# Kernel optimization log

Measured on AMD Instinct MI355X. Metric: run time of the kernel, lower is better.

## Reference

```python
import jax, jax.numpy as jnp
import numpy as np

B, N, K, G = 8, 2048, 20, 8
EPS = 1e-5

def lrelu(v):
    return jnp.where(v >= 0, v, 0.2 * v)

def group_norm(x, gamma, beta):
    # x: (B, C, ...); normalize over channel groups and spatial dims
    b, c = x.shape[0], x.shape[1]
    xg = x.reshape(b, G, c // G, -1)
    mu = xg.mean(axis=(2, 3), keepdims=True)
    var = xg.var(axis=(2, 3), keepdims=True)
    xn = ((xg - mu) * jax.lax.rsqrt(var + EPS)).reshape(x.shape)
    sh = (1, c) + (1,) * (x.ndim - 2)
    return xn * gamma.reshape(sh) + beta.reshape(sh)

def graph_feature(x, k):
    # x: (B, C, N) -> edge features (B, 2C, N, k)
    inner = 2.0 * jnp.einsum('bcn,bcm->bnm', x, x)
    xx = jnp.sum(x * x, axis=1)                     # (B, N)
    pd = -(xx[:, :, None] - inner + xx[:, None, :]) # negative squared dist
    idx = jax.lax.top_k(pd, k)[1]                   # (B, N, k) nearest
    xt = jnp.swapaxes(x, 1, 2)                      # (B, N, C)
    nbr = jax.vmap(lambda f, i: f[i])(xt, idx)      # (B, N, k, C) gather
    ctr = jnp.broadcast_to(xt[:, :, None, :], nbr.shape)
    feat = jnp.concatenate([nbr - ctr, ctr], axis=-1)  # (B, N, k, 2C)
    return jnp.transpose(feat, (0, 3, 1, 2))

def edge_block(x, w, b, g, h):
    f = graph_feature(x, K)
    y = jnp.einsum('oc,bcnk->bonk', w, f) + b[None, :, None, None]
    return lrelu(group_norm(y, g, h)).max(axis=-1)   # (B, out, N)

def _forward(x, w0, b0, g0, h0, w1, b1, g1, h1, w2, b2, g2, h2,
             w3, b3, g3, h3, fw0, fb0, fw1, fb1, fw2, fb2):
    cur = jnp.swapaxes(x, 1, 2)                      # (B, 3, N)
    res = []
    for (w, b, g, h) in ((w0, b0, g0, h0), (w1, b1, g1, h1), (w2, b2, g2, h2)):
        cur = edge_block(cur, w, b, g, h)
        res.append(cur)
    xc = jnp.concatenate(res, axis=1)                # (B, 256, N)
    pf = jnp.einsum('oc,bcn->bon', w3, xc) + b3[None, :, None]
    pf = lrelu(group_norm(pf, g3, h3))               # (B, 256, N)
    v = jnp.concatenate([pf.max(axis=-1), pf.mean(axis=-1)], axis=1)  # (B, 512)
    v = lrelu(v @ fw0.T + fb0)
    v = lrelu(v @ fw1.T + fb1)
    return v @ fw2.T + fb2                           # (B, 256)

def setup_inputs():
    key = jax.random.key(0)
    ks = jax.random.split(key, 16)
    def rn(k, shape, s=0.05):
        return jax.random.normal(k, shape, jnp.float32) * s
    inp = {'x': jax.random.normal(ks[0], (B, N, 3), jnp.float32)}
    inp.update(w0=rn(ks[1], (64, 6)), b0=rn(ks[2], (64,)), g0=jnp.ones((64,)), h0=jnp.zeros((64,)))
    inp.update(w1=rn(ks[3], (64, 128)), b1=rn(ks[4], (64,)), g1=jnp.ones((64,)), h1=jnp.zeros((64,)))
    inp.update(w2=rn(ks[5], (128, 128)), b2=rn(ks[6], (128,)), g2=jnp.ones((128,)), h2=jnp.zeros((128,)))
    inp.update(w3=rn(ks[7], (256, 256)), b3=rn(ks[8], (256,)), g3=jnp.ones((256,)), h3=jnp.zeros((256,)))
    inp.update(fw0=rn(ks[9], (512, 512)), fb0=rn(ks[10], (512,)))
    inp.update(fw1=rn(ks[11], (512, 512)), fb1=rn(ks[12], (512,)))
    inp.update(fw2=rn(ks[13], (256, 512)), fb2=rn(ks[14], (256,)))
    return inp

def reference(x, w0, b0, g0, h0, w1, b1, g1, h1, w2, b2, g2, h2,
              w3, b3, g3, h3, fw0, fb0, fw1, fb1, fw2, fb2):
    return _forward(x, w0, b0, g0, h0, w1, b1, g1, h1, w2, b2, g2, h2,
                    w3, b3, g3, h3, fw0, fb0, fw1, fb1, fw2, fb2)
```

## Files before the change

### kernel.cpp

```cpp
#include <hip/hip_runtime.h>
#include <hip/hip_bf16.h>
#include <cstdint>


constexpr int B = 8, N = 2048, KNN = 20, G = 8;
constexpr int BN = B * N;
constexpr float EPS = 1e-5f;

using bf16 = __hip_bfloat16;
using u64 = unsigned long long;

__device__ __forceinline__ float lrelu(float v){ return v >= 0.f ? v : 0.2f * v; }
__device__ __forceinline__ unsigned fenc(float f){ unsigned u = __float_as_uint(f); return (u & 0x80000000u) ? ~u : (u | 0x80000000u); }
__device__ __forceinline__ float fdec(unsigned u){ return (u & 0x80000000u) ? __uint_as_float(u & 0x7FFFFFFFu) : __uint_as_float(~u); }

template<int NB>
__device__ __forceinline__ void batcher_sort(unsigned* s){
  #pragma unroll
  for (int p = 1; p < NB; p <<= 1){
    #pragma unroll
    for (int k = p; k >= 1; k >>= 1){
      #pragma unroll
      for (int j = k % p; j <= NB-1-k; j += 2*k){
        #pragma unroll
        for (int i = 0; i <= ((k-1 < NB-1-j-k) ? k-1 : NB-1-j-k); ++i){
          if ((i + j) / (2*p) == (i + j + k) / (2*p)){
            const unsigned lo = min(s[i+j], s[i+j+k]);
            const unsigned hi = max(s[i+j], s[i+j+k]);
            s[i+j] = lo; s[i+j+k] = hi;
          }
        }
      }
    }
  }
}

template<int NB>
__device__ __forceinline__ void topk_update(unsigned* L, const unsigned* s){
  #pragma unroll
  for (int i = 0; i < NB; ++i) L[i] = min(L[i], s[i]);
  #pragma unroll
  for (int gap = 16; gap >= 1; gap >>= 1){
    #pragma unroll
    for (int i = 0; i < 32; ++i){
      if ((i & ((gap<<1)-1)) < gap){
        const unsigned hi = max(L[i], L[i+gap]);
        const unsigned lo = min(L[i], L[i+gap]);
        L[i] = hi; L[i+gap] = lo;
      }
    }
  }
}

__device__ __forceinline__ u64 knn_dec8(unsigned kk, int q){
  const unsigned ord = kk & 255u;
  const unsigned gidx = (ord >> 4)*128u + (unsigned)q + 8u*(ord & 15u);
  return ((u64)(kk & 0xFFFFFF00u) << 24) | gidx;
}

__device__ __forceinline__ void knn_merge32(unsigned char* ovl, const unsigned* L,
    int* __restrict__ knn_out, size_t bp, int r0, int sr, int sq){
  unsigned* mbuf = (unsigned*)ovl;
  #pragma unroll
  for (int k = 0; k < KNN; ++k) mbuf[(sr*8 + sq)*KNN + k] = L[31-k];
  __syncthreads();
  if (sq == 0){
    int h[8]; u64 v[8];
    #pragma unroll
    for (int q = 0; q < 8; ++q){ h[q] = 0; v[q] = knn_dec8(mbuf[(sr*8+q)*KNN], q); }
    int* outp = &knn_out[(bp + r0 + sr)*KNN];
    for (int k = 0; k < KNN; ++k){
      int best = 0; u64 bv = v[0];
      #pragma unroll
      for (int q = 1; q < 8; ++q) if (v[q] < bv){ bv = v[q]; best = q; }
      outp[k] = (int)(unsigned)(bv & 0xFFFFu);
      #pragma unroll
      for (int q = 0; q < 8; ++q) if (q == best){
        ++h[q];
        v[q] = (h[q] < KNN) ? knn_dec8(mbuf[(sr*8+q)*KNN + h[q]], q) : ~0ULL;
      }
    }
  }
}

struct SrcPtrs { const void* p[23]; };

__global__ __launch_bounds__(256) void convert_kernel(SrcPtrs sp, float* __restrict__ dst,
                                                      float* gstat, unsigned* vmax, float* vmean){
  if (blockIdx.y == 23){
    int t = blockIdx.x * 256 + threadIdx.x;
    if (t < 512) gstat[t] = 0.f;
    if (t < B*256){ vmax[t] = 0x007FFFFFu; vmean[t] = 0.f; }
    return;
  }
  constexpr int CNT[23] = {49152,384,64,64,64,8192,64,64,64,16384,128,128,128,
                           65536,256,256,256,262144,512,262144,512,131072,256};
  constexpr int OFF[23] = {0,49152,49536,49600,49664,49728,57920,57984,58048,58112,
                           74496,74624,74752,74880,140416,140672,140928,141184,
                           403328,403840,665984,666496,797568};
  const int ti = blockIdx.y;
  const int cnt = CNT[ti], off = OFF[ti];
  const unsigned g0w = *(const unsigned*)sp.p[3];
  const bool isbf = (g0w & 0xFFFFu) == 0x3F80u;
  const float* fs = (const float*)sp.p[ti];
  const unsigned short* bs = (const unsigned short*)sp.p[ti];
  for (int j = blockIdx.x*256 + threadIdx.x; j < cnt; j += gridDim.x*256){
    dst[off + j] = isbf ? __uint_as_float((unsigned)bs[j] << 16) : fs[j];
  }
}

template<int C>
__global__ __launch_bounds__(256) void sqnorm_cm(const float* __restrict__ f, float* __restrict__ cn){
  const int p = blockIdx.x*256 + threadIdx.x;
  float s = 0.f;
  #pragma unroll 8
  for (int c = 0; c < C; ++c){ const float v = f[(size_t)c*BN + p]; s += v*v; }
  cn[p] = s;
}

template<int C>
__global__ __launch_bounds__(256) void knn_kernel(const float* __restrict__ feat, const float* __restrict__ cnG,
                                                  int* __restrict__ knn_out){
  constexpr int ROWS = 32, CT = 128, DTP = 133;
  constexpr int COLF_BYTES = C*CT*4;
  constexpr int MERGE_BYTES = ROWS*8*KNN*4;
  constexpr int OVL = COLF_BYTES + ROWS*DTP*4;
  __shared__ __align__(16) unsigned char ovl[OVL];
  __shared__ __align__(16) float rowfT[C][ROWS];
  float* colfT = (float*)ovl;
  float* dbuf  = (float*)(ovl + COLF_BYTES);

  const int t = threadIdx.x;
  const int b = blockIdx.y;
  const int r0 = blockIdx.x * ROWS;
  const size_t bp = (size_t)b * N;
  const int rg = (t & 7)*4;
  const int cg = (t >> 3)*4;
  const int sr = t >> 3;
  const int sq = t & 7;
  const float rn = cnG[bp + r0 + sr];

  for (int i = t; i < C*(ROWS/4); i += 256){
    const int c = i >> 3, r4 = (i & 7)*4;
    *(float4*)&rowfT[c][r4] = *(const float4*)&feat[(size_t)c*BN + bp + r0 + r4];
  }

  unsigned L[32];
  #pragma unroll
  for (int k = 0; k < 32; ++k) L[k] = 0xFFFFFFFFu;

  for (int ct = 0; ct < N/CT; ++ct){
    const int m0 = ct * CT;
    __syncthreads();
    for (int i = t; i < C*(CT/4); i += 256){
      const int c = i >> 5, m4 = (i & 31)*4;
      *(float4*)&colfT[c*CT + m4] = *(const float4*)&feat[(size_t)c*BN + bp + m0 + m4];
    }
    const float4 cn4 = *(const float4*)&cnG[bp + m0 + cg];
    __syncthreads();

    float acc[4][4];
    #pragma unroll
    for (int i=0;i<4;i++){
      #pragma unroll
      for (int j=0;j<4;j++) acc[i][j]=0.f; }
    for (int c = 0; c < C; ++c){
      float4 ar = *(const float4*)&rowfT[c][rg];
      float4 cl = *(const float4*)&colfT[c*CT + cg];
      acc[0][0]+=ar.x*cl.x; acc[0][1]+=ar.x*cl.y; acc[0][2]+=ar.x*cl.z; acc[0][3]+=ar.x*cl.w;
      acc[1][0]+=ar.y*cl.x; acc[1][1]+=ar.y*cl.y; acc[1][2]+=ar.y*cl.z; acc[1][3]+=ar.y*cl.w;
      acc[2][0]+=ar.z*cl.x; acc[2][1]+=ar.z*cl.y; acc[2][2]+=ar.z*cl.z; acc[2][3]+=ar.z*cl.w;
      acc[3][0]+=ar.w*cl.x; acc[3][1]+=ar.w*cl.y; acc[3][2]+=ar.w*cl.z; acc[3][3]+=ar.w*cl.w;
    }
    #pragma unroll
    for (int i=0;i<4;i++){
      float4 s;
      s.x = cn4.x - 2.f*acc[i][0]; s.y = cn4.y - 2.f*acc[i][1];
      s.z = cn4.z - 2.f*acc[i][2]; s.w = cn4.w - 2.f*acc[i][3];
      *(float4*)&dbuf[(rg+i)*DTP + cg] = s;
    }
    __syncthreads();

    const float* drow = &dbuf[sr*DTP];
    unsigned s16[16];
    #pragma unroll
    for (int j = 0; j < 16; ++j){
      const float d = fmaxf(drow[sq + 8*j] + rn, 0.f);
      s16[j] = (__float_as_uint(d) & 0xFFFFFF00u) | (unsigned)(ct*16 + j);
    }
    batcher_sort<16>(s16);
    topk_update<16>(L, s16);
  }

  __syncthreads();
  knn_merge32(ovl, L, knn_out, bp, r0, sr, sq);
}

__global__ __launch_bounds__(256) void knn3_kernel(const float* __restrict__ x, int* __restrict__ knn_out){
  constexpr int ROWS = 32, CT = 128;
  constexpr int MERGE_BYTES = ROWS*8*KNN*4;
  __shared__ __align__(16) unsigned char ovl[MERGE_BYTES];
  float* cx = (float*)ovl;
  float* cy = cx + CT;
  float* cz = cy + CT;

  const int t = threadIdx.x;
  const int b = blockIdx.y;
  const int r0 = blockIdx.x * ROWS;
  const size_t bp = (size_t)b * N;
  const int sr = t >> 3, sq = t & 7;
  const float rx = x[(bp + r0 + sr)*3 + 0];
  const float ry = x[(bp + r0 + sr)*3 + 1];
  const float rz = x[(bp + r0 + sr)*3 + 2];

  unsigned L[32];
  #pragma unroll
  for (int k = 0; k < 32; ++k) L[k] = 0xFFFFFFFFu;

  for (int ct = 0; ct < N/CT; ++ct){
    __syncthreads();
    if (t < CT){
      const size_t q = (bp + ct*CT + t)*3;
      cx[t] = x[q]; cy[t] = x[q+1]; cz[t] = x[q+2];
    }
    __syncthreads();
    unsigned s16[16];
    #pragma unroll
    for (int j = 0; j < 16; ++j){
      const int m = sq + 8*j;
      const float dx = rx - cx[m], dy = ry - cy[m], dz = rz - cz[m];
      const float d = dx*dx + dy*dy + dz*dz;
      s16[j] = (__float_as_uint(d) & 0xFFFFFF00u) | (unsigned)(ct*16 + j);
    }
    batcher_sort<16>(s16);
    topk_update<16>(L, s16);
  }

  __syncthreads();
  knn_merge32(ovl, L, knn_out, bp, r0, sr, sq);
}

template<int C, int COUT, int MT, bool CM>
__global__ __launch_bounds__(256) void zu_kernel(const float* __restrict__ feat, const float* __restrict__ w,
                                                 const float* __restrict__ bias,
                                                 float* __restrict__ z, float* __restrict__ u){
  __shared__ __align__(16) float fT[C][MT+4];
  __shared__ __align__(16) float Wt[C][COUT+4];
  const int t = threadIdx.x;
  const size_t p0 = (size_t)blockIdx.x * MT;
  if constexpr (CM){
    for (int i = t; i < C*(MT/4); i += 256){
      const int c = i / (MT/4), m4 = (i % (MT/4))*4;
      float4 v = *(const float4*)&feat[(size_t)c*BN + p0 + m4];
      *(float4*)&fT[c][m4] = v;
    }
  } else {
    for (int i = t; i < MT*C; i += 256){ int m = i / C, c = i - m*C; fT[c][m] = feat[(p0+m)*C + c]; }
  }
  for (int i = t; i < COUT*C; i += 256){ int o = i / C, c = i - o*C; Wt[c][o] = w[o*(2*C) + c]; }
  __syncthreads();
  constexpr int MQ = MT/4;
  const int rq = t % MQ, oq = t / MQ;
  const int mm = rq*4, oo = oq*8;
  float acc[4][8];
  #pragma unroll
  for (int i=0;i<4;i++){
    #pragma unroll
    for (int j=0;j<8;j++) acc[i][j] = 0.f; }
  for (int c = 0; c < C; ++c){
    float fr[4], wv[8];
    { float4 v = *(const float4*)&fT[c][mm]; fr[0]=v.x; fr[1]=v.y; fr[2]=v.z; fr[3]=v.w; }
    { float4 v = *(const float4*)&Wt[c][oo];   wv[0]=v.x; wv[1]=v.y; wv[2]=v.z; wv[3]=v.w; }
    { float4 v = *(const float4*)&Wt[c][oo+4]; wv[4]=v.x; wv[5]=v.y; wv[6]=v.z; wv[7]=v.w; }
    #pragma unroll
    for (int i=0;i<4;i++){
      #pragma unroll
      for (int j=0;j<8;j++) acc[i][j] += fr[i]*wv[j];
    }
  }
  #pragma unroll
  for (int i=0;i<4;i++){
    float4 s0, s1;
    s0.x=acc[i][0]; s0.y=acc[i][1]; s0.z=acc[i][2]; s0.w=acc[i][3];
    s1.x=acc[i][4]; s1.y=acc[i][5]; s1.z=acc[i][6]; s1.w=acc[i][7];
    *(float4*)&z[(p0+mm+i)*COUT + oo]     = s0;
    *(float4*)&z[(p0+mm+i)*COUT + oo + 4] = s1;
  }
  __syncthreads();
  for (int i = t; i < COUT*C; i += 256){
    int o = i / C, c = i - o*C;
    Wt[c][o] = w[o*2*C + C + c] - w[o*2*C + c];
  }
  __syncthreads();
  #pragma unroll
  for (int i=0;i<4;i++){
    #pragma unroll
    for (int j=0;j<8;j++) acc[i][j] = 0.f; }
  for (int c = 0; c < C; ++c){
    float fr[4], wv[8];
    { float4 v = *(const float4*)&fT[c][mm]; fr[0]=v.x; fr[1]=v.y; fr[2]=v.z; fr[3]=v.w; }
    { float4 v = *(const float4*)&Wt[c][oo];   wv[0]=v.x; wv[1]=v.y; wv[2]=v.z; wv[3]=v.w; }
    { float4 v = *(const float4*)&Wt[c][oo+4]; wv[4]=v.x; wv[5]=v.y; wv[6]=v.z; wv[7]=v.w; }
    #pragma unroll
    for (int i=0;i<4;i++){
      #pragma unroll
      for (int j=0;j<8;j++) acc[i][j] += fr[i]*wv[j];
    }
  }
  float bb[8];
  #pragma unroll
  for (int j=0;j<8;j++) bb[j] = bias[oo+j];
  #pragma unroll
  for (int i=0;i<4;i++){
    float4 s0, s1;
    s0.x=acc[i][0]+bb[0]; s0.y=acc[i][1]+bb[1]; s0.z=acc[i][2]+bb[2]; s0.w=acc[i][3]+bb[3];
    s1.x=acc[i][4]+bb[4]; s1.y=acc[i][5]+bb[5]; s1.z=acc[i][6]+bb[6]; s1.w=acc[i][7]+bb[7];
    *(float4*)&u[(p0+mm+i)*COUT + oo]     = s0;
    *(float4*)&u[(p0+mm+i)*COUT + oo + 4] = s1;
  }
}

template<int COUT, bool MM>
__global__ __launch_bounds__(256) void edge_stats_kernel(const float* __restrict__ z, const float* __restrict__ u,
                                                         const int* __restrict__ knn, float* __restrict__ gstat,
                                                         float* __restrict__ emax, float* __restrict__ emin){
  constexpr int REPS = 256 / COUT;
  constexpr int PPT  = 16 / REPS;
  __shared__ float red[G*2];
  const int t = threadIdx.x;
  const int o = t % COUT, pr = t / COUT;
  const size_t base = (size_t)blockIdx.x * 16;
  const int b = (int)(base / N);
  if (t < G*2) red[t] = 0.f;
  __syncthreads();
  float s1 = 0.f, s2 = 0.f;
  for (int j = 0; j < PPT; ++j){
    const size_t p = base + pr + (size_t)j*REPS;
    const float uu = u[p*COUT + o];
    const int* kn = knn + p*KNN;
    float mx = -3.0e38f, mn = 3.0e38f;
    for (int k = 0; k < KNN; ++k){
      const int m = kn[k];
      const float y = z[((size_t)b*N + m)*COUT + o] + uu;
      s1 += y; s2 += y*y;
      mx = fmaxf(mx, y); mn = fminf(mn, y);
    }
    if constexpr (MM){
      emax[(size_t)o*BN + p] = mx;
      emin[(size_t)o*BN + p] = mn;
    }
  }
  const int g = o / (COUT/G);
  atomicAdd(&red[g*2+0], s1);
  atomicAdd(&red[g*2+1], s2);
  __syncthreads();
  if (t < G*2) atomicAdd(&gstat[b*(G*2) + t], red[t]);
}

template<int COUT>
__global__ __launch_bounds__(256) void edge_norm_mm(const float* __restrict__ emax, const float* __restrict__ emin,
    const float* __restrict__ gstat, const float* __restrict__ gamma, const float* __restrict__ beta,
    float* __restrict__ fout, float cntInv){
  const int o = blockIdx.y;
  const int p = blockIdx.x*1024 + threadIdx.x*4;
  const int b = p >> 11;
  const int g = o / (COUT/G);
  const float s1 = gstat[b*(G*2) + g*2 + 0];
  const float s2 = gstat[b*(G*2) + g*2 + 1];
  const float mu  = s1 * cntInv;
  const float var = s2 * cntInv - mu*mu;
  const float inv = rsqrtf(var + EPS);
  const float sc = gamma[o] * inv;
  const float sh = beta[o] - mu * sc;
  float4 mx = *(const float4*)&emax[(size_t)o*BN + p];
  float4 mn = *(const float4*)&emin[(size_t)o*BN + p];
  float4 r;
  r.x = lrelu(sc*(sc>=0.f?mx.x:mn.x)+sh);
  r.y = lrelu(sc*(sc>=0.f?mx.y:mn.y)+sh);
  r.z = lrelu(sc*(sc>=0.f?mx.z:mn.z)+sh);
  r.w = lrelu(sc*(sc>=0.f?mx.w:mn.w)+sh);
  *(float4*)&fout[(size_t)o*BN + p] = r;
}

template<int COUT>
__global__ __launch_bounds__(256) void edge_norm_kernel(const float* __restrict__ z, const float* __restrict__ u,
    const int* __restrict__ knn, const float* __restrict__ gstat,
    const float* __restrict__ gamma, const float* __restrict__ beta,
    float* __restrict__ fout, float cntInv){
  constexpr int REPS = 256 / COUT;
  constexpr int PPT  = 16 / REPS;
  const int t = threadIdx.x;
  const int o = t % COUT, pr = t / COUT;
  const size_t base = (size_t)blockIdx.x * 16;
  const int b = (int)(base / N);
  const int g = o / (COUT/G);
  const float s1 = gstat[b*(G*2) + g*2 + 0];
  const float s2 = gstat[b*(G*2) + g*2 + 1];
  const float mu  = s1 * cntInv;
  const float var = s2 * cntInv - mu*mu;
  const float inv = rsqrtf(var + EPS);
  const float sc = gamma[o] * inv;
  const float sh = beta[o] - mu * sc;
  for (int j = 0; j < PPT; ++j){
    const size_t p = base + pr + (size_t)j*REPS;
    const float uu = u[p*COUT + o];
    const int* kn = knn + p*KNN;
    float mx = -3.0e38f;
    for (int k = 0; k < KNN; ++k){
      const int m = kn[k];
      const float y = z[((size_t)b*N + m)*COUT + o] + uu;
      mx = fmaxf(mx, lrelu(sc*y + sh));
    }
    fout[(size_t)o*BN + p] = mx;
  }
}

__global__ __launch_bounds__(256) void conv3_kernel(const float* __restrict__ f1, const float* __restrict__ f2,
    const float* __restrict__ f3, const float* __restrict__ w3, const float* __restrict__ b3,
    float* __restrict__ y3, float* __restrict__ gstat){
  __shared__ __align__(16) float fT[32][64+4];
  __shared__ __align__(16) float Wt[32][256+4];
  __shared__ float red[G*2];
  const int t = threadIdx.x;
  const size_t p0 = (size_t)blockIdx.x * 64;
  const int b = (int)(p0 / N);
  const int rq = t & 15, oq = t >> 4;
  const int mm = rq*4, oo = oq*16;
  if (t < G*2) red[t] = 0.f;
  float acc[4][16];
  #pragma unroll
  for (int i=0;i<4;i++){
    #pragma unroll
    for (int j=0;j<16;j++) acc[i][j] = 0.f; }
  for (int cc = 0; cc < 8; ++cc){
    __syncthreads();
    const float* src; int coff;
    if (cc < 2){ src = f1; coff = cc*32; }
    else if (cc < 4){ src = f2; coff = (cc-2)*32; }
    else { src = f3; coff = (cc-4)*32; }
    for (int i = t; i < 512; i += 256){
      const int c = i >> 4, m4 = (i & 15)*4;
      float4 v = *(const float4*)&src[(size_t)(coff+c)*BN + p0 + m4];
      *(float4*)&fT[c][m4] = v;
    }
    for (int i = t; i < 2048; i += 256){
      int o = i >> 3, cq = (i & 7)*4;
      float4 v = *(const float4*)&w3[(size_t)o*256 + cc*32 + cq];
      Wt[cq+0][o]=v.x; Wt[cq+1][o]=v.y; Wt[cq+2][o]=v.z; Wt[cq+3][o]=v.w;
    }
    __syncthreads();
    for (int c = 0; c < 32; ++c){
      float fr[4], wv[16];
      { float4 v = *(const float4*)&fT[c][mm]; fr[0]=v.x; fr[1]=v.y; fr[2]=v.z; fr[3]=v.w; }
      { float4 v = *(const float4*)&Wt[c][oo+0];  wv[0]=v.x;  wv[1]=v.y;  wv[2]=v.z;  wv[3]=v.w;  }
      { float4 v = *(const float4*)&Wt[c][oo+4];  wv[4]=v.x;  wv[5]=v.y;  wv[6]=v.z;  wv[7]=v.w;  }
      { float4 v = *(const float4*)&Wt[c][oo+8];  wv[8]=v.x;  wv[9]=v.y;  wv[10]=v.z; wv[11]=v.w; }
      { float4 v = *(const float4*)&Wt[c][oo+12]; wv[12]=v.x; wv[13]=v.y; wv[14]=v.z; wv[15]=v.w; }
      #pragma unroll
      for (int i=0;i<4;i++){
        #pragma unroll
        for (int j=0;j<16;j++) acc[i][j] += fr[i]*wv[j];
      }
    }
  }
  float bb[16];
  #pragma unroll
  for (int j=0;j<16;j++) bb[j] = b3[oo+j];
  float s1 = 0.f, s2 = 0.f;
  #pragma unroll
  for (int i=0;i<4;i++){
    #pragma unroll
    for (int j=0;j<16;j++){
      acc[i][j] += bb[j];
      s1 += acc[i][j]; s2 += acc[i][j]*acc[i][j];
    }
  }
  #pragma unroll
  for (int i=0;i<4;i++){
    #pragma unroll
    for (int q=0;q<4;q++){
      float4 s;
      s.x=acc[i][q*4+0]; s.y=acc[i][q*4+1]; s.z=acc[i][q*4+2]; s.w=acc[i][q*4+3];
      *(float4*)&y3[(p0+mm+i)*256 + oo + q*4] = s;
    }
  }
  const int g = oo >> 5;
  atomicAdd(&red[g*2+0], s1);
  atomicAdd(&red[g*2+1], s2);
  __syncthreads();
  if (t < G*2) atomicAdd(&gstat[b*(G*2) + t], red[t]);
}

__global__ __launch_bounds__(256) void pf_kernel(const float* __restrict__ y3, const float* __restrict__ gstat,
    const float* __restrict__ g3, const float* __restrict__ h3,
    unsigned* __restrict__ vmax, float* __restrict__ vmean){
  const int o = threadIdx.x;
  const int b = blockIdx.y;
  const int n0 = blockIdx.x * 64;
  const int g = o >> 5;
  const float cntInv = 1.f/(32.f*N);
  const float s1 = gstat[b*(G*2)+g*2+0], s2 = gstat[b*(G*2)+g*2+1];
  const float mu = s1*cntInv, var = s2*cntInv - mu*mu;
  const float inv = rsqrtf(var + EPS);
  const float sc = g3[o] * inv;
  const float sh = h3[o] - mu*sc;
  float mx = -3.0e38f, sm = 0.f;
  for (int n = n0; n < n0+64; ++n){
    float v = y3[((size_t)b*N + n)*256 + o];
    v = lrelu(sc*v + sh);
    mx = fmaxf(mx, v);
    sm += v;
  }
  atomicMax(&vmax[b*256+o], fenc(mx));
  atomicAdd(&vmean[b*256+o], sm * (1.f/N));
}

__global__ __launch_bounds__(256) void fc_fused(const unsigned* __restrict__ vmax, const float* __restrict__ vmean,
    const float* __restrict__ fw0, const float* __restrict__ fb0,
    const float* __restrict__ fw1, const float* __restrict__ fb1,
    const float* __restrict__ fw2, const float* __restrict__ fb2,
    void* outp, const unsigned* __restrict__ dflag){
  __shared__ float va[512], vb[512];
  const int t = threadIdx.x, b = blockIdx.x;
  for (int c = t; c < 512; c += 256)
    va[c] = (c < 256) ? fdec(vmax[b*256 + c]) : vmean[b*256 + (c-256)];
  __syncthreads();
  {
    float a0 = fb0[t], a1 = fb0[t+256];
    const float* w0p = fw0 + (size_t)t*512;
    const float* w1p = fw0 + (size_t)(t+256)*512;
    for (int c = 0; c < 512; c += 4){
      float4 wa = *(const float4*)&w0p[c];
      float4 wb = *(const float4*)&w1p[c];
      a0 += wa.x*va[c+0] + wa.y*va[c+1] + wa.z*va[c+2] + wa.w*va[c+3];
      a1 += wb.x*va[c+0] + wb.y*va[c+1] + wb.z*va[c+2] + wb.w*va[c+3];
    }
    vb[t] = lrelu(a0); vb[t+256] = lrelu(a1);
  }
  __syncthreads();
  {
    float a0 = fb1[t], a1 = fb1[t+256];
    const float* w0p = fw1 + (size_t)t*512;
    const float* w1p = fw1 + (size_t)(t+256)*512;
    for (int c = 0; c < 512; c += 4){
      float4 wa = *(const float4*)&w0p[c];
      float4 wb = *(const float4*)&w1p[c];
      a0 += wa.x*vb[c+0] + wa.y*vb[c+1] + wa.z*vb[c+2] + wa.w*vb[c+3];
      a1 += wb.x*vb[c+0] + wb.y*vb[c+1] + wb.z*vb[c+2] + wb.w*vb[c+3];
    }
    va[t] = lrelu(a0); va[t+256] = lrelu(a1);
  }
  __syncthreads();
  {
    float a = fb2[t];
    const float* wp = fw2 + (size_t)t*512;
    for (int c = 0; c < 512; c += 4){
      float4 wv = *(const float4*)&wp[c];
      a += wv.x*va[c+0] + wv.y*va[c+1] + wv.z*va[c+2] + wv.w*va[c+3];
    }
    const bool isbf = ((*dflag) & 0xFFFFu) == 0x3F80u;
    if (isbf) ((bf16*)outp)[b*256 + t] = __float2bfloat16(a);
    else      ((float*)outp)[b*256 + t] = a;
  }
}

extern "C" void kernel_launch(void* const* d_in, const int* in_sizes, int n_in,
                              void* d_out, int out_size, void* d_ws, size_t ws_size,
                              hipStream_t stream){
  (void)in_sizes; (void)n_in; (void)out_size;

  float* ws = (float*)d_ws;
  float* f1 = ws;
  float* f2 = f1 + (size_t)64*BN;
  float* f3 = f2 + (size_t)64*BN;
  float* zb = f3 + (size_t)128*BN;
  float* ub = zb + (size_t)128*BN;
  int*   kn = (int*)(ub + (size_t)128*BN);
  float* gs = (float*)(kn + (size_t)BN*KNN);
  unsigned* vmax = (unsigned*)(gs + 512);
  float* vmean = (float*)(vmax + B*256);
  float* cnG = vmean + B*256;
  float* pc = cnG + (size_t)BN;
  float* y3 = zb;
  float* emax2 = pc + 797824;
  float* emin2 = emax2 + (size_t)128*BN;
  const size_t need2 = (size_t)((emin2 + (size_t)128*BN) - ws) * 4;
  const bool fused2 = (ws_size >= need2);
  float* emax01 = f3;
  float* emin01 = f3 + (size_t)64*BN;

  const float* xc  = pc + 0;
  const float* w0c = pc + 49152;  const float* b0c = pc + 49536;
  const float* g0c = pc + 49600;  const float* h0c = pc + 49664;
  const float* w1c = pc + 49728;  const float* b1c = pc + 57920;
  const float* g1c = pc + 57984;  const float* h1c = pc + 58048;
  const float* w2c = pc + 58112;  const float* b2c = pc + 74496;
  const float* g2c = pc + 74624;  const float* h2c = pc + 74752;
  const float* w3c = pc + 74880;  const float* b3c = pc + 140416;
  const float* g3c = pc + 140672; const float* h3c = pc + 140928;
  const float* fw0c= pc + 141184; const float* fb0c= pc + 403328;
  const float* fw1c= pc + 403840; const float* fb1c= pc + 665984;
  const float* fw2c= pc + 666496; const float* fb2c= pc + 797568;

  SrcPtrs sp;
  for (int i = 0; i < 23; ++i) sp.p[i] = d_in[i];
  convert_kernel<<<dim3(64, 24), 256, 0, stream>>>(sp, pc, gs, vmax, vmean);

  knn3_kernel<<<dim3(N/32, B), 256, 0, stream>>>(xc, kn);
  zu_kernel<3, 64, 128, false><<<BN/128, 256, 0, stream>>>(xc, w0c, b0c, zb, ub);
  edge_stats_kernel<64,true><<<BN/16, 256, 0, stream>>>(zb, ub, kn, gs + 0, emax01, emin01);
  edge_norm_mm<64><<<dim3(BN/1024, 64), 256, 0, stream>>>(emax01, emin01, gs + 0, g0c, h0c, f1, 1.f/327680.f);

  sqnorm_cm<64><<<BN/256, 256, 0, stream>>>(f1, cnG);
  knn_kernel<64><<<dim3(N/32, B), 256, 0, stream>>>(f1, cnG, kn);
  zu_kernel<64, 64, 128, true><<<BN/128, 256, 0, stream>>>(f1, w1c, b1c, zb, ub);
  edge_stats_kernel<64,true><<<BN/16, 256, 0, stream>>>(zb, ub, kn, gs + 128, emax01, emin01);
  edge_norm_mm<64><<<dim3(BN/1024, 64), 256, 0, stream>>>(emax01, emin01, gs + 128, g1c, h1c, f2, 1.f/327680.f);

  sqnorm_cm<64><<<BN/256, 256, 0, stream>>>(f2, cnG);
  knn_kernel<64><<<dim3(N/32, B), 256, 0, stream>>>(f2, cnG, kn);
  zu_kernel<64, 128, 64, true><<<BN/64, 256, 0, stream>>>(f2, w2c, b2c, zb, ub);
  if (fused2){
    edge_stats_kernel<128,true><<<BN/16, 256, 0, stream>>>(zb, ub, kn, gs + 256, emax2, emin2);
    edge_norm_mm<128><<<dim3(BN/1024, 128), 256, 0, stream>>>(emax2, emin2, gs + 256, g2c, h2c, f3, 1.f/655360.f);
  } else {
    edge_stats_kernel<128,false><<<BN/16, 256, 0, stream>>>(zb, ub, kn, gs + 256, nullptr, nullptr);
    edge_norm_kernel<128><<<BN/16, 256, 0, stream>>>(zb, ub, kn, gs + 256, g2c, h2c, f3, 1.f/655360.f);
  }

  conv3_kernel<<<BN/64, 256, 0, stream>>>(f1, f2, f3, w3c, b3c, y3, gs + 384);
  pf_kernel<<<dim3(32, B), 256, 0, stream>>>(y3, gs + 384, g3c, h3c, vmax, vmean);

  fc_fused<<<B, 256, 0, stream>>>(vmax, vmean, fw0c, fb0c, fw1c, fb1c, fw2c, fb2c,
                                  d_out, (const unsigned*)d_in[3]);
}
```

Before: 703.5 us.

## Store edge max/min point-major and transpose in norm kernels; alias knn smem

Edge stats now write emax/emin point-major (p*COUT+o), so per-thread channel writes coalesce. A new tiled edge_norm_t64 transposes back to channel-major through shared memory for layers 1–2. Layer 3 stays point-major via edge_norm_rm, and conv3 reads f3 with a transposing load. Separately, knn_kernel aliases the distance buffer onto the column-feature buffer, which needs an extra barrier; this cuts LDS use to allow higher occupancy.

```diff
diff --git a/kernel.cpp b/kernel.cpp
--- a/kernel.cpp
+++ b/kernel.cpp
@@ -123,12 +123,10 @@
                                                   int* __restrict__ knn_out){
   constexpr int ROWS = 32, CT = 128, DTP = 133;
   constexpr int COLF_BYTES = C*CT*4;
-  constexpr int MERGE_BYTES = ROWS*8*KNN*4;
-  constexpr int OVL = COLF_BYTES + ROWS*DTP*4;
-  __shared__ __align__(16) unsigned char ovl[OVL];
+  __shared__ __align__(16) unsigned char ovl[COLF_BYTES];
   __shared__ __align__(16) float rowfT[C][ROWS];
   float* colfT = (float*)ovl;
-  float* dbuf  = (float*)(ovl + COLF_BYTES);
+  float* dbuf  = (float*)ovl;
 
   const int t = threadIdx.x;
   const int b = blockIdx.y;
@@ -172,6 +170,7 @@
       acc[2][0]+=ar.z*cl.x; acc[2][1]+=ar.z*cl.y; acc[2][2]+=ar.z*cl.z; acc[2][3]+=ar.z*cl.w;
       acc[3][0]+=ar.w*cl.x; acc[3][1]+=ar.w*cl.y; acc[3][2]+=ar.w*cl.z; acc[3][3]+=ar.w*cl.w;
     }
+    __syncthreads();
     #pragma unroll
     for (int i=0;i<4;i++){
       float4 s;
@@ -346,8 +345,8 @@
       mx = fmaxf(mx, y); mn = fminf(mn, y);
     }
     if constexpr (MM){
-      emax[(size_t)o*BN + p] = mx;
-      emin[(size_t)o*BN + p] = mn;
+      emax[p*COUT + o] = mx;
+      emin[p*COUT + o] = mn;
     }
   }
   const int g = o / (COUT/G);
@@ -357,29 +356,70 @@
   if (t < G*2) atomicAdd(&gstat[b*(G*2) + t], red[t]);
 }
 
-template<int COUT>
-__global__ __launch_bounds__(256) void edge_norm_mm(const float* __restrict__ emax, const float* __restrict__ emin,
+__global__ __launch_bounds__(256) void edge_norm_t64(const float* __restrict__ emax, const float* __restrict__ emin,
     const float* __restrict__ gstat, const float* __restrict__ gamma, const float* __restrict__ beta,
     float* __restrict__ fout, float cntInv){
-  const int o = blockIdx.y;
-  const int p = blockIdx.x*1024 + threadIdx.x*4;
-  const int b = p >> 11;
+  __shared__ float tile[64][68];
+  const int t = threadIdx.x;
+  const size_t p0 = (size_t)blockIdx.x * 64;
+  const int b = (int)(p0 / N);
+  const int o4 = (t & 15) * 4;
+  float sc[4], sh[4];
+  #pragma unroll
+  for (int e = 0; e < 4; ++e){
+    const int o = o4 + e;
+    const int g = o >> 3;
+    const float s1 = gstat[b*16 + g*2+0], s2 = gstat[b*16 + g*2+1];
+    const float mu = s1*cntInv, var = s2*cntInv - mu*mu;
+    const float inv = rsqrtf(var + EPS);
+    sc[e] = gamma[o]*inv; sh[e] = beta[o] - mu*sc[e];
+  }
+  #pragma unroll
+  for (int j = 0; j < 4; ++j){
+    const int p = (t >> 4) + 16*j;
+    float4 mx = *(const float4*)&emax[(p0+p)*64 + o4];
+    float4 mn = *(const float4*)&emin[(p0+p)*64 + o4];
+    float4 r;
+    r.x = lrelu(sc[0]*(sc[0]>=0.f?mx.x:mn.x)+sh[0]);
+    r.y = lrelu(sc[1]*(sc[1]>=0.f?mx.y:mn.y)+sh[1]);
+    r.z = lrelu(sc[2]*(sc[2]>=0.f?mx.z:mn.z)+sh[2]);
+    r.w = lrelu(sc[3]*(sc[3]>=0.f?mx.w:mn.w)+sh[3]);
+    *(float4*)&tile[p][o4] = r;
+  }
+  __syncthreads();
+  const int o = t >> 2;
+  #pragma unroll
+  for (int jj = 0; jj < 4; ++jj){
+    const int p = (t & 3)*4 + 16*jj;
+    float4 r;
+    r.x = tile[p+0][o]; r.y = tile[p+1][o]; r.z = tile[p+2][o]; r.w = tile[p+3][o];
+    *(float4*)&fout[(size_t)o*BN + p0 + p] = r;
+  }
+}
+
+template<int COUT>
+__global__ __launch_bounds__(256) void edge_norm_rm(const float* __restrict__ emax, const float* __restrict__ emin,
+    const float* __restrict__ gstat, const float* __restrict__ gamma, const float* __restrict__ beta,
+    float* __restrict__ fout, float cntInv){
+  const size_t base = ((size_t)blockIdx.x*256 + threadIdx.x)*4;
+  const int o = (int)(base & (COUT-1));
+  const int b = (int)(base / ((size_t)N*COUT));
   const int g = o / (COUT/G);
   const float s1 = gstat[b*(G*2) + g*2 + 0];
   const float s2 = gstat[b*(G*2) + g*2 + 1];
   const float mu  = s1 * cntInv;
   const float var = s2 * cntInv - mu*mu;
   const float inv = rsqrtf(var + EPS);
-  const float sc = gamma[o] * inv;
-  const float sh = beta[o] - mu * sc;
-  float4 mx = *(const float4*)&emax[(size_t)o*BN + p];
-  float4 mn = *(const float4*)&emin[(size_t)o*BN + p];
+  float4 gm = *(const float4*)&gamma[o];
+  float4 bt = *(const float4*)&beta[o];
+  float4 mx = *(const float4*)&emax[base];
+  float4 mn = *(const float4*)&emin[base];
   float4 r;
-  r.x = lrelu(sc*(sc>=0.f?mx.x:mn.x)+sh);
-  r.y = lrelu(sc*(sc>=0.f?mx.y:mn.y)+sh);
-  r.z = lrelu(sc*(sc>=0.f?mx.z:mn.z)+sh);
-  r.w = lrelu(sc*(sc>=0.f?mx.w:mn.w)+sh);
-  *(float4*)&fout[(size_t)o*BN + p] = r;
+  { const float sc = gm.x*inv, sh = bt.x - mu*sc; r.x = lrelu(sc*(sc>=0.f?mx.x:mn.x)+sh); }
+  { const float sc = gm.y*inv, sh = bt.y - mu*sc; r.y = lrelu(sc*(sc>=0.f?mx.y:mn.y)+sh); }
+  { const float sc = gm.z*inv, sh = bt.z - mu*sc; r.z = lrelu(sc*(sc>=0.f?mx.z:mn.z)+sh); }
+  { const float sc = gm.w*inv, sh = bt.w - mu*sc; r.w = lrelu(sc*(sc>=0.f?mx.w:mn.w)+sh); }
+  *(float4*)&fout[base] = r;
 }
 
 template<int COUT>
@@ -411,7 +451,7 @@
       const float y = z[((size_t)b*N + m)*COUT + o] + uu;
       mx = fmaxf(mx, lrelu(sc*y + sh));
     }
-    fout[(size_t)o*BN + p] = mx;
+    fout[p*COUT + o] = mx;
   }
 }
 
@@ -434,14 +474,21 @@
     for (int j=0;j<16;j++) acc[i][j] = 0.f; }
   for (int cc = 0; cc < 8; ++cc){
     __syncthreads();
-    const float* src; int coff;
-    if (cc < 2){ src = f1; coff = cc*32; }
-    else if (cc < 4){ src = f2; coff = (cc-2)*32; }
-    else { src = f3; coff = (cc-4)*32; }
-    for (int i = t; i < 512; i += 256){
-      const int c = i >> 4, m4 = (i & 15)*4;
-      float4 v = *(const float4*)&src[(size_t)(coff+c)*BN + p0 + m4];
-      *(float4*)&fT[c][m4] = v;
+    if (cc < 4){
+      const float* src = (cc < 2) ? f1 : f2;
+      const int coff = (cc & 1)*32;
+      for (int i = t; i < 512; i += 256){
+        const int c = i >> 4, m4 = (i & 15)*4;
+        float4 v = *(const float4*)&src[(size_t)(coff+c)*BN + p0 + m4];
+        *(float4*)&fT[c][m4] = v;
+      }
+    } else {
+      const int coff = (cc-4)*32;
+      for (int i = t; i < 512; i += 256){
+        const int m = i >> 3, cq = (i & 7)*4;
+        float4 v = *(const float4*)&f3[(p0+m)*128 + coff + cq];
+        fT[cq+0][m]=v.x; fT[cq+1][m]=v.y; fT[cq+2][m]=v.z; fT[cq+3][m]=v.w;
+      }
     }
     for (int i = t; i < 2048; i += 256){
       int o = i >> 3, cq = (i & 7)*4;
@@ -609,20 +656,20 @@
   knn3_kernel<<<dim3(N/32, B), 256, 0, stream>>>(xc, kn);
   zu_kernel<3, 64, 128, false><<<BN/128, 256, 0, stream>>>(xc, w0c, b0c, zb, ub);
   edge_stats_kernel<64,true><<<BN/16, 256, 0, stream>>>(zb, ub, kn, gs + 0, emax01, emin01);
-  edge_norm_mm<64><<<dim3(BN/1024, 64), 256, 0, stream>>>(emax01, emin01, gs + 0, g0c, h0c, f1, 1.f/327680.f);
+  edge_norm_t64<<<BN/64, 256, 0, stream>>>(emax01, emin01, gs + 0, g0c, h0c, f1, 1.f/327680.f);
 
   sqnorm_cm<64><<<BN/256, 256, 0, stream>>>(f1, cnG);
   knn_kernel<64><<<dim3(N/32, B), 256, 0, stream>>>(f1, cnG, kn);
   zu_kernel<64, 64, 128, true><<<BN/128, 256, 0, stream>>>(f1, w1c, b1c, zb, ub);
   edge_stats_kernel<64,true><<<BN/16, 256, 0, stream>>>(zb, ub, kn, gs + 128, emax01, emin01);
-  edge_norm_mm<64><<<dim3(BN/1024, 64), 256, 0, stream>>>(emax01, emin01, gs + 128, g1c, h1c, f2, 1.f/327680.f);
+  edge_norm_t64<<<BN/64, 256, 0, stream>>>(emax01, emin01, gs + 128, g1c, h1c, f2, 1.f/327680.f);
 
   sqnorm_cm<64><<<BN/256, 256, 0, stream>>>(f2, cnG);
   knn_kernel<64><<<dim3(N/32, B), 256, 0, stream>>>(f2, cnG, kn);
   zu_kernel<64, 128, 64, true><<<BN/64, 256, 0, stream>>>(f2, w2c, b2c, zb, ub);
   if (fused2){
     edge_stats_kernel<128,true><<<BN/16, 256, 0, stream>>>(zb, ub, kn, gs + 256, emax2, emin2);
-    edge_norm_mm<128><<<dim3(BN/1024, 128), 256, 0, stream>>>(emax2, emin2, gs + 256, g2c, h2c, f3, 1.f/655360.f);
+    edge_norm_rm<128><<<(BN*128)/1024, 256, 0, stream>>>(emax2, emin2, gs + 256, g2c, h2c, f3, 1.f/655360.f);
   } else {
     edge_stats_kernel<128,false><<<BN/16, 256, 0, stream>>>(zb, ub, kn, gs + 256, nullptr, nullptr);
     edge_norm_kernel<128><<<BN/16, 256, 0, stream>>>(zb, ub, kn, gs + 256, g2c, h2c, f3, 1.f/655360.f);
```

Measured after the change: 679.5 us. 3.4% less time.
